# Kernel optimization log

Measured on AMD Instinct MI355X. Metric: run time of the kernel, lower is better.

Reference implementation:

```python
import jax, jax.numpy as jnp
import numpy as np

NU = 100000  # user nodes
NI = 100000  # item nodes
NE = 600000  # edges per etype


def mean_agg(Wh, src, dst, n_dst):
    # copy_u + mean reduce: gather projected src feats, segment-mean over dst
    msg = Wh[src]                                               # [E, d]
    s = jax.ops.segment_sum(msg, dst, num_segments=n_dst)       # [n_dst, d]
    deg = jax.ops.segment_sum(jnp.ones((src.shape[0],), Wh.dtype), dst,
                              num_segments=n_dst)               # [n_dst]
    return s / jnp.maximum(deg, 1.0)[:, None]                   # isolated nodes -> 0


def setup_inputs() -> dict:
    key = jax.random.key(0)
    ks = jax.random.split(key, 20)
    d_in, d_hid, d_out = 128, 128, 16
    inp = {
        'embed_user': jax.random.normal(ks[0], (NU, d_in), jnp.float32),
        'embed_item': jax.random.normal(ks[1], (NI, d_in), jnp.float32),
        'src_uu': jax.random.randint(ks[2], (NE,), 0, NU, jnp.int32),
        'dst_uu': jax.random.randint(ks[3], (NE,), 0, NU, jnp.int32),
        'src_ui': jax.random.randint(ks[4], (NE,), 0, NU, jnp.int32),
        'dst_ui': jax.random.randint(ks[5], (NE,), 0, NI, jnp.int32),
        'src_iu': jax.random.randint(ks[6], (NE,), 0, NI, jnp.int32),
        'dst_iu': jax.random.randint(ks[7], (NE,), 0, NU, jnp.int32),
        'W0_uu': jax.random.normal(ks[8], (d_in, d_hid), jnp.float32) * 0.05,
        'b0_uu': jax.random.normal(ks[9], (d_hid,), jnp.float32) * 0.05,
        'W0_ui': jax.random.normal(ks[10], (d_in, d_hid), jnp.float32) * 0.05,
        'b0_ui': jax.random.normal(ks[11], (d_hid,), jnp.float32) * 0.05,
        'W0_iu': jax.random.normal(ks[12], (d_in, d_hid), jnp.float32) * 0.05,
        'b0_iu': jax.random.normal(ks[13], (d_hid,), jnp.float32) * 0.05,
        'W1_uu': jax.random.normal(ks[14], (d_hid, d_out), jnp.float32) * 0.05,
        'b1_uu': jax.random.normal(ks[15], (d_out,), jnp.float32) * 0.05,
        'W1_ui': jax.random.normal(ks[16], (d_hid, d_out), jnp.float32) * 0.05,
        'b1_ui': jax.random.normal(ks[17], (d_out,), jnp.float32) * 0.05,
        'W1_iu': jax.random.normal(ks[18], (d_hid, d_out), jnp.float32) * 0.05,
        'b1_iu': jax.random.normal(ks[19], (d_out,), jnp.float32) * 0.05,
    }
    return inp


def reference(embed_user, embed_item,
              src_uu, dst_uu, src_ui, dst_ui, src_iu, dst_iu,
              W0_uu, b0_uu, W0_ui, b0_ui, W0_iu, b0_iu,
              W1_uu, b1_uu, W1_ui, b1_ui, W1_iu, b1_iu):
    # Layer 0: per-etype linear, copy_u+mean per etype, sum-combine per dst ntype
    h_user = (mean_agg(embed_user @ W0_uu + b0_uu, src_uu, dst_uu, NU)
              + mean_agg(embed_item @ W0_iu + b0_iu, src_iu, dst_iu, NU))
    h_item = mean_agg(embed_user @ W0_ui + b0_ui, src_ui, dst_ui, NI)
    h_user = jax.nn.relu(h_user)
    h_item = jax.nn.relu(h_item)
    # Layer 1 (dropout p=0): only category='user' output is returned
    out = (mean_agg(h_user @ W1_uu + b1_uu, src_uu, dst_uu, NU)
           + mean_agg(h_item @ W1_iu + b1_iu, src_iu, dst_iu, NU))
    return out
```

## Files before the change

### kernel.cpp

```cpp
#include <hip/hip_runtime.h>
#include <hip/hip_bf16.h>

#define NU 100000
#define NI 100000
#define NEDGE 600000
#define DIN 128
#define DOUT 16
#define NPAD 100032
#define BSH 9
#define NBUCK 196
#define NSB 256
#define SCH 2344

typedef __attribute__((ext_vector_type(8))) short short8;
typedef __attribute__((ext_vector_type(4))) float f32x4;

#define W_EU   0ull
#define W_AUI  6400000ull
#define W_AUU  12802048ull
#define W_AIU  19204096ull
#define W_PW   25606144ull
#define W_OFFU 25632768ull
#define W_OFFI 25732784ull
#define W_OFFX 25832800ull
#define W_SUU  25932816ull
#define W_SIU  26532816ull
#define W_SUI  27132816ull
#define W_EI   27732944ull
#define WS_FULL_BYTES (34132944ull * 4)

__device__ inline unsigned pack_bf16(float x, float y) {
  __hip_bfloat162 h = __float22bfloat162_rn(make_float2(x, y));
  unsigned u;
  __builtin_memcpy(&u, &h, 4);
  return u;
}

__device__ inline short bf16_bits(float x) {
  __hip_bfloat16 h = __float2bfloat16(x);
  short s;
  __builtin_memcpy(&s, &h, 2);
  return s;
}

__device__ inline void bf2_accw(unsigned u, float w, float& ax, float& ay) {
  unsigned lo = u << 16, hi = u & 0xffff0000u;
  float f0, f1;
  __builtin_memcpy(&f0, &lo, 4);
  __builtin_memcpy(&f1, &hi, 4);
  ax = fmaf(f0, w, ax);
  ay = fmaf(f1, w, ay);
}

__global__ __launch_bounds__(256) void prep_kernel(
    const float* __restrict__ Eu, const float* __restrict__ Ei,
    unsigned* __restrict__ Eu_b, unsigned* __restrict__ Ei_b,
    const int* __restrict__ d_uu, const int* __restrict__ d_iu, const int* __restrict__ d_ui,
    int* __restrict__ M,
    const float* __restrict__ W0_uu, const float* __restrict__ W0_ui,
    const float* __restrict__ W0_iu, const float* __restrict__ W1_uu,
    const float* __restrict__ W1_iu, short* __restrict__ pW0_uu, short* __restrict__ pW0_ui,
    short* __restrict__ pW0_iu, short* __restrict__ pW1_uu, short* __restrict__ pW1_iu,
    int nconvU, int nconvI) {
  __shared__ int h[NBUCK];
  int b = blockIdx.x;
  int tid = threadIdx.x;
  if (b < nconvU + nconvI) {
    const float* src;
    unsigned* dst;
    int t;
    if (b < nconvU) { src = Eu; dst = Eu_b; t = b * 256 + tid; }
    else { src = Ei; dst = Ei_b; t = (b - nconvU) * 256 + tid; }
    const float4* s4 = (const float4*)src;
    float4 x = s4[(size_t)t * 2], y = s4[(size_t)t * 2 + 1];
    uint4 o;
    o.x = pack_bf16(x.x, x.y);
    o.y = pack_bf16(x.z, x.w);
    o.z = pack_bf16(y.x, y.y);
    o.w = pack_bf16(y.z, y.w);
    ((uint4*)dst)[t] = o;
    return;
  }
  b -= nconvU + nconvI;
  if (b < 3 * NSB) {
    int t = b / NSB, k = b % NSB;
    if (tid < NBUCK) h[tid] = 0;
    __syncthreads();
    const int* d = (t == 0) ? d_uu : (t == 1) ? d_iu : d_ui;
    int e0 = k * SCH, e1 = min(e0 + SCH, NEDGE);
    for (int e = e0 + tid; e < e1; e += 256) atomicAdd(&h[d[e] >> BSH], 1);
    __syncthreads();
    if (tid < NBUCK) M[t * (NBUCK * NSB) + tid * NSB + k] = h[tid];
    return;
  }
  b -= 3 * NSB;
  int t = b * 256 + tid;
  const float* src;
  short* dst;
  int base;
  bool w1 = false;
  if (t < 16384) { src = W0_uu; dst = pW0_uu; base = t; }
  else if (t < 32768) { src = W0_ui; dst = pW0_ui; base = t - 16384; }
  else if (t < 49152) { src = W0_iu; dst = pW0_iu; base = t - 32768; }
  else if (t < 51200) { src = W1_uu; dst = pW1_uu; base = t - 49152; w1 = true; }
  else if (t < 53248) { src = W1_iu; dst = pW1_iu; base = t - 51200; w1 = true; }
  else return;
  int j = base & 7;
  int lane = (base >> 3) & 63;
  int frag = base >> 9;
  int quad = lane >> 4, l16 = lane & 15;
  float val;
  if (!w1) {
    int kc = frag >> 3, nt = frag & 7;
    val = src[(kc * 32 + quad * 8 + j) * 128 + nt * 16 + l16];
  } else {
    int kc = frag;
    val = src[(kc * 32 + quad * 8 + j) * 16 + l16];
  }
  dst[base] = bf16_bits(val);
}

__global__ __launch_bounds__(256) void scanM_kernel(int* __restrict__ M,
                                                    int* __restrict__ Btot) {
  int t = blockIdx.x / NBUCK, b = blockIdx.x % NBUCK;
  int* Mt = M + t * (NBUCK * NSB) + b * NSB;
  __shared__ int wls[4];
  __shared__ int tot;
  int tid = threadIdx.x, lane = tid & 63, wv = tid >> 6;
  int v = Mt[tid];
  int x = v;
#pragma unroll
  for (int d = 1; d < 64; d <<= 1) {
    int y = __shfl_up(x, d, 64);
    if (lane >= d) x += y;
  }
  if (lane == 63) wls[wv] = x;
  __syncthreads();
  if (tid == 0) {
    int r = 0;
#pragma unroll
    for (int i = 0; i < 4; i++) { int tt = wls[i]; wls[i] = r; r += tt; }
    tot = r;
  }
  __syncthreads();
  Mt[tid] = x - v + wls[wv];
  if (tid == 0) Btot[t * NBUCK + b] = tot;
}

__global__ __launch_bounds__(256) void scanB_kernel(const int* __restrict__ Btot,
                                                    int* __restrict__ Bbase) {
  int t = blockIdx.x;
  __shared__ int wls[4];
  int tid = threadIdx.x, lane = tid & 63, wv = tid >> 6;
  int v = (tid < NBUCK) ? Btot[t * NBUCK + tid] : 0;
  int x = v;
#pragma unroll
  for (int d = 1; d < 64; d <<= 1) {
    int y = __shfl_up(x, d, 64);
    if (lane >= d) x += y;
  }
  if (lane == 63) wls[wv] = x;
  __syncthreads();
  if (tid == 0) {
    int r = 0;
#pragma unroll
    for (int i = 0; i < 4; i++) { int tt = wls[i]; wls[i] = r; r += tt; }
  }
  __syncthreads();
  if (tid < NBUCK) Bbase[t * NBUCK + tid] = x - v + wls[wv];
}

__global__ __launch_bounds__(256) void coarse_scatter_kernel(
    const int* __restrict__ s_uu, const int* __restrict__ d_uu,
    const int* __restrict__ s_iu, const int* __restrict__ d_iu,
    const int* __restrict__ s_ui, const int* __restrict__ d_ui,
    const int* __restrict__ M, const int* __restrict__ Bbase, uint2* __restrict__ pairs) {
  __shared__ int cur[NBUCK];
  int t = blockIdx.x / NSB, k = blockIdx.x % NSB;
  int tid = threadIdx.x;
  if (tid < NBUCK) cur[tid] = M[t * (NBUCK * NSB) + tid * NSB + k] + Bbase[t * NBUCK + tid];
  __syncthreads();
  const int* src = (t == 0) ? s_uu : (t == 1) ? s_iu : s_ui;
  const int* dst = (t == 0) ? d_uu : (t == 1) ? d_iu : d_ui;
  uint2* pr = pairs + (size_t)t * NEDGE;
  int e0 = k * SCH, e1 = min(e0 + SCH, NEDGE);
  for (int e = e0 + tid; e < e1; e += 256) {
    int d = dst[e];
    int pos = atomicAdd(&cur[d >> BSH], 1);
    pr[pos] = make_uint2((unsigned)src[e], (unsigned)d);
  }
}

__global__ __launch_bounds__(256) void fine_sort_kernel(
    const uint2* __restrict__ pairs, const int* __restrict__ Bbase,
    const int* __restrict__ Btot,
    int* __restrict__ off_uu, int* __restrict__ off_iu, int* __restrict__ off_ui,
    int* __restrict__ ssrc_uu, int* __restrict__ ssrc_iu, int* __restrict__ ssrc_ui) {
  __shared__ int h[1 << BSH];
  __shared__ int wls[4];
  int t = blockIdx.x / NBUCK, b = blockIdx.x % NBUCK;
  int tid = threadIdx.x, lane = tid & 63, wv = tid >> 6;
  int* off = (t == 0) ? off_uu : (t == 1) ? off_iu : off_ui;
  int* ss = (t == 0) ? ssrc_uu : (t == 1) ? ssrc_iu : ssrc_ui;
  const uint2* pr = pairs + (size_t)t * NEDGE;
  int base = b << BSH;
  int base_off = Bbase[t * NBUCK + b];
  int cnt = Btot[t * NBUCK + b];
  h[tid] = 0;
  h[tid + 256] = 0;
  __syncthreads();
  for (int e = base_off + tid; e < base_off + cnt; e += 256)
    atomicAdd(&h[(int)pr[e].y - base], 1);
  __syncthreads();
  int h0 = h[2 * tid], h1 = h[2 * tid + 1];
  int s = h0 + h1, x = s;
#pragma unroll
  for (int d = 1; d < 64; d <<= 1) {
    int y = __shfl_up(x, d, 64);
    if (lane >= d) x += y;
  }
  if (lane == 63) wls[wv] = x;
  __syncthreads();
  if (tid == 0) {
    int r = 0;
#pragma unroll
    for (int i = 0; i < 4; i++) { int tt = wls[i]; wls[i] = r; r += tt; }
  }
  __syncthreads();
  int excl = base_off + x - s + wls[wv];
  h[2 * tid] = excl;
  h[2 * tid + 1] = excl + h0;
  __syncthreads();
  int nn = min(1 << BSH, NU - base);
  for (int i = tid; i < nn; i += 256) off[base + i] = h[i];
  if (b == NBUCK - 1 && tid == 0) off[NU] = base_off + cnt;
  __syncthreads();
  for (int e = base_off + tid; e < base_off + cnt; e += 256) {
    uint2 p = pr[e];
    int pos = atomicAdd(&h[(int)p.y - base], 1);
    ss[pos] = (int)p.x;
  }
}

__global__ __launch_bounds__(64, 4) void fused_layer_kernel(
    const uint4* __restrict__ Xu4, const void* __restrict__ Xi, int xi_bf16,
    const int* __restrict__ off_ui, const int* __restrict__ off_uu, const int* __restrict__ off_iu,
    const int* __restrict__ s_ui, const int* __restrict__ s_uu, const int* __restrict__ s_iu,
    const short* __restrict__ pW0_ui, const short* __restrict__ pW0_uu,
    const short* __restrict__ pW0_iu, const float* __restrict__ b0_ui,
    const float* __restrict__ b0_uu, const float* __restrict__ b0_iu,
    const short* __restrict__ pW1_iu, const short* __restrict__ pW1_uu,
    const float* __restrict__ b1_iu, const float* __restrict__ b1_uu,
    float* __restrict__ P_iu, float* __restrict__ P_uu, int nbi) {
  __shared__ __align__(16) float hs[2560];

  const int lane = threadIdx.x;
  const bool user = (int)blockIdx.x < nbi;
  const int blk = user ? (int)blockIdx.x : (int)blockIdx.x - nbi;
  const int rb = blk * 16;

  float* hw = &hs[0];
  uint4* A0 = (uint4*)hw;
  uint4* A1 = A0 + 256;

  {
    const int g = lane >> 4, l16 = lane & 15;
    const int npass = user ? 2 : 1;
#pragma unroll 1
    for (int pass = 0; pass < npass; pass++) {
      const int* off = pass ? off_iu : (user ? off_uu : off_ui);
      const int* ss = pass ? s_iu : (user ? s_uu : s_ui);
      uint4* A = pass ? A1 : A0;
      const bool bf = pass ? (xi_bf16 != 0) : true;
      const uint4* X = pass ? (const uint4*)Xi : Xu4;
      const float4* Xf = (const float4*)Xi;
      if (bf) {
#pragma unroll 1
        for (int ip = 0; ip < 2; ip++) {
          int rA = g * 4 + ip * 2, rB = rA + 1;
          int nodeA = rb + rA, nodeB = rb + rB;
          float acA[8], acB[8];
#pragma unroll
          for (int j = 0; j < 8; j++) { acA[j] = 0.f; acB[j] = 0.f; }
          int s0A = 0, s1A = 0, s0B = 0, s1B = 0;
          if (nodeA < NU) { s0A = off[nodeA]; s1A = off[nodeA + 1]; }
          if (nodeB < NU) { s0B = off[nodeB]; s1B = off[nodeB + 1]; }
          int degA = s1A - s0A, degB = s1B - s0B;
#pragma unroll 1
          for (int eA = s0A, eB = s0B; eA < s1A || eB < s1B; eA += 8, eB += 8) {
            int idxA[8], idxB[8];
            float wtA[8], wtB[8];
#pragma unroll
            for (int j = 0; j < 8; j++) {
              int ea = eA + j, eb = eB + j;
              wtA[j] = (ea < s1A) ? 1.f : 0.f;
              wtB[j] = (eb < s1B) ? 1.f : 0.f;
              idxA[j] = ss[max(min(ea, s1A - 1), 0)];
              idxB[j] = ss[max(min(eb, s1B - 1), 0)];
            }
            uint4 vA[8], vB[8];
#pragma unroll
            for (int j = 0; j < 8; j++) vA[j] = X[(size_t)idxA[j] * 16 + l16];
#pragma unroll
            for (int j = 0; j < 8; j++) vB[j] = X[(size_t)idxB[j] * 16 + l16];
#pragma unroll
            for (int j = 0; j < 8; j++) {
              bf2_accw(vA[j].x, wtA[j], acA[0], acA[1]);
              bf2_accw(vA[j].y, wtA[j], acA[2], acA[3]);
              bf2_accw(vA[j].z, wtA[j], acA[4], acA[5]);
              bf2_accw(vA[j].w, wtA[j], acA[6], acA[7]);
            }
#pragma unroll
            for (int j = 0; j < 8; j++) {
              bf2_accw(vB[j].x, wtB[j], acB[0], acB[1]);
              bf2_accw(vB[j].y, wtB[j], acB[2], acB[3]);
              bf2_accw(vB[j].z, wtB[j], acB[4], acB[5]);
              bf2_accw(vB[j].w, wtB[j], acB[6], acB[7]);
            }
          }
          float invA = 1.0f / fmaxf((float)degA, 1.0f);
          float invB = 1.0f / fmaxf((float)degB, 1.0f);
          uint4 oA, oB;
          oA.x = pack_bf16(acA[0] * invA, acA[1] * invA);
          oA.y = pack_bf16(acA[2] * invA, acA[3] * invA);
          oA.z = pack_bf16(acA[4] * invA, acA[5] * invA);
          oA.w = pack_bf16(acA[6] * invA, acA[7] * invA);
          oB.x = pack_bf16(acB[0] * invB, acB[1] * invB);
          oB.y = pack_bf16(acB[2] * invB, acB[3] * invB);
          oB.z = pack_bf16(acB[4] * invB, acB[5] * invB);
          oB.w = pack_bf16(acB[6] * invB, acB[7] * invB);
          A[rA * 16 + (l16 ^ (rA & 7))] = oA;
          A[rB * 16 + (l16 ^ (rB & 7))] = oB;
        }
      } else {
#pragma unroll 1
        for (int it = 0; it < 4; it++) {
          int r = g * 4 + it;
          int node = rb + r;
          float ac[8];
#pragma unroll
          for (int j = 0; j < 8; j++) ac[j] = 0.f;
          int deg = 0;
          if (node < NU) {
            int s0 = off[node], s1 = off[node + 1];
            deg = s1 - s0;
            if (deg > 0) {
              for (int e = s0; e < s1; e += 4) {
                int idx[4];
                float wt[4];
#pragma unroll
                for (int j = 0; j < 4; j++) {
                  int ee = e + j;
                  bool v = ee < s1;
                  idx[j] = ss[v ? ee : s1 - 1];
                  wt[j] = v ? 1.f : 0.f;
                }
#pragma unroll
                for (int j = 0; j < 4; j++) {
                  float4 pa = Xf[(size_t)idx[j] * 32 + l16 * 2];
                  float4 qa = Xf[(size_t)idx[j] * 32 + l16 * 2 + 1];
                  ac[0] = fmaf(pa.x, wt[j], ac[0]); ac[1] = fmaf(pa.y, wt[j], ac[1]);
                  ac[2] = fmaf(pa.z, wt[j], ac[2]); ac[3] = fmaf(pa.w, wt[j], ac[3]);
                  ac[4] = fmaf(qa.x, wt[j], ac[4]); ac[5] = fmaf(qa.y, wt[j], ac[5]);
                  ac[6] = fmaf(qa.z, wt[j], ac[6]); ac[7] = fmaf(qa.w, wt[j], ac[7]);
                }
              }
            }
          }
          float inv = 1.0f / fmaxf((float)deg, 1.0f);
          uint4 o;
          o.x = pack_bf16(ac[0] * inv, ac[1] * inv);
          o.y = pack_bf16(ac[2] * inv, ac[3] * inv);
          o.z = pack_bf16(ac[4] * inv, ac[5] * inv);
          o.w = pack_bf16(ac[6] * inv, ac[7] * inv);
          A[r * 16 + (l16 ^ (r & 7))] = o;
        }
      }
    }
  }

  const short8* B0p = (const short8*)(user ? pW0_uu : pW0_ui);
  short8 b0pre[8];
#pragma unroll
  for (int nt = 0; nt < 8; nt++) b0pre[nt] = B0p[nt * 64 + lane];

  __syncthreads();

  const int quad = lane >> 4, q16 = lane & 15;
  const int* off0 = user ? off_uu : off_ui;
  const float* b0a = user ? b0_uu : b0_ui;
  const short* W1p = user ? pW1_uu : pW1_iu;
  const float* b1v = user ? b1_uu : b1_iu;
  float* P = user ? P_uu : P_iu;

  float m0[4], m1[4];
#pragma unroll
  for (int r = 0; r < 4; r++) {
    int rr = rb + quad * 4 + r;
    m0[r] = 0.f;
    m1[r] = 0.f;
    if (rr < NU) {
      m0[r] = (off0[rr + 1] > off0[rr]) ? 1.f : 0.f;
      if (user) m1[r] = (off_iu[rr + 1] > off_iu[rr]) ? 1.f : 0.f;
    }
  }

  f32x4 acc[8];
#pragma unroll
  for (int nt = 0; nt < 8; nt++) {
    float ba = b0a[nt * 16 + q16];
    float bb = user ? b0_iu[nt * 16 + q16] : 0.f;
#pragma unroll
    for (int r = 0; r < 4; r++) acc[nt][r] = ba * m0[r] + bb * m1[r];
  }

  const short8* B1p = (const short8*)pW0_iu;
  union u4s8 { uint4 u; short8 s; };
#pragma unroll
  for (int kc = 0; kc < 4; kc++) {
    int c = kc * 4 + quad;
    u4s8 a0, a1;
    a0.u = A0[q16 * 16 + (c ^ (q16 & 7))];
    if (user) a1.u = A1[q16 * 16 + (c ^ (q16 & 7))];
#pragma unroll
    for (int nt = 0; nt < 8; nt++) {
      short8 b0 = (kc == 0) ? b0pre[nt] : B0p[(kc * 8 + nt) * 64 + lane];
      acc[nt] = __builtin_amdgcn_mfma_f32_16x16x32_bf16(a0.s, b0, acc[nt], 0, 0, 0);
      if (user) {
        short8 bb = B1p[(kc * 8 + nt) * 64 + lane];
        acc[nt] = __builtin_amdgcn_mfma_f32_16x16x32_bf16(a1.s, bb, acc[nt], 0, 0, 0);
      }
    }
  }
  __syncthreads();

#pragma unroll
  for (int nt = 0; nt < 8; nt++) {
    int col = nt * 16 + q16;
    float4 v;
    v.x = fmaxf(acc[nt][0], 0.f);
    v.y = fmaxf(acc[nt][1], 0.f);
    v.z = fmaxf(acc[nt][2], 0.f);
    v.w = fmaxf(acc[nt][3], 0.f);
    *(float4*)&hw[col * 20 + quad * 4] = v;
  }
  __syncthreads();

  f32x4 acc2;
  {
    float bv = b1v[q16];
    acc2[0] = bv; acc2[1] = bv; acc2[2] = bv; acc2[3] = bv;
  }
  const short8* W1f = (const short8*)W1p;
#pragma unroll
  for (int kc = 0; kc < 4; kc++) {
    float f[8];
#pragma unroll
    for (int j = 0; j < 8; j++) f[j] = hw[(kc * 32 + quad * 8 + j) * 20 + q16];
    union { uint4 u; short8 s; } hf;
    hf.u.x = pack_bf16(f[0], f[1]);
    hf.u.y = pack_bf16(f[2], f[3]);
    hf.u.z = pack_bf16(f[4], f[5]);
    hf.u.w = pack_bf16(f[6], f[7]);
    short8 bw = W1f[kc * 64 + lane];
    acc2 = __builtin_amdgcn_mfma_f32_16x16x32_bf16(hf.s, bw, acc2, 0, 0, 0);
  }
#pragma unroll
  for (int r = 0; r < 4; r++) {
    int rr = rb + quad * 4 + r;
    if (rr < NU) P[(size_t)rr * DOUT + q16] = acc2[r];
  }
}

__global__ __launch_bounds__(256) void out_kernel(const float4* __restrict__ P_uu,
                                                  const float4* __restrict__ P_iu,
                                                  const int* __restrict__ off_uu,
                                                  const int* __restrict__ s_uu,
                                                  const int* __restrict__ off_iu,
                                                  const int* __restrict__ s_iu,
                                                  float4* __restrict__ out) {
  int w = threadIdx.x >> 6, lane = threadIdx.x & 63;
  int q = lane & 3;
  int sl = (lane >> 2) & 3;
  int nl = lane >> 4;
  int node = blockIdx.x * 16 + w * 4 + nl;
  float4 a = make_float4(0.f, 0.f, 0.f, 0.f);
  float4 b = a;
  int s0 = off_uu[node], s1 = off_uu[node + 1];
  for (int e = s0 + sl; e < s1; e += 16) {
    int idx[4];
    float wt[4];
#pragma unroll
    for (int j = 0; j < 4; j++) {
      int ee = e + j * 4;
      bool v = ee < s1;
      idx[j] = s_uu[v ? ee : s1 - 1];
      wt[j] = v ? 1.f : 0.f;
    }
    float4 vv[4];
#pragma unroll
    for (int j = 0; j < 4; j++) vv[j] = P_uu[(size_t)idx[j] * 4 + q];
#pragma unroll
    for (int j = 0; j < 4; j++) {
      a.x = fmaf(vv[j].x, wt[j], a.x); a.y = fmaf(vv[j].y, wt[j], a.y);
      a.z = fmaf(vv[j].z, wt[j], a.z); a.w = fmaf(vv[j].w, wt[j], a.w);
    }
  }
  int t0 = off_iu[node], t1 = off_iu[node + 1];
  for (int e = t0 + sl; e < t1; e += 16) {
    int idx[4];
    float wt[4];
#pragma unroll
    for (int j = 0; j < 4; j++) {
      int ee = e + j * 4;
      bool v = ee < t1;
      idx[j] = s_iu[v ? ee : t1 - 1];
      wt[j] = v ? 1.f : 0.f;
    }
    float4 vv[4];
#pragma unroll
    for (int j = 0; j < 4; j++) vv[j] = P_iu[(size_t)idx[j] * 4 + q];
#pragma unroll
    for (int j = 0; j < 4; j++) {
      b.x = fmaf(vv[j].x, wt[j], b.x); b.y = fmaf(vv[j].y, wt[j], b.y);
      b.z = fmaf(vv[j].z, wt[j], b.z); b.w = fmaf(vv[j].w, wt[j], b.w);
    }
  }
  float ia = 1.0f / fmaxf((float)(s1 - s0), 1.0f);
  float ib = 1.0f / fmaxf((float)(t1 - t0), 1.0f);
  float4 r;
  r.x = a.x * ia + b.x * ib;
  r.y = a.y * ia + b.y * ib;
  r.z = a.z * ia + b.z * ib;
  r.w = a.w * ia + b.w * ib;
  r.x += __shfl_xor(r.x, 4, 64); r.y += __shfl_xor(r.y, 4, 64);
  r.z += __shfl_xor(r.z, 4, 64); r.w += __shfl_xor(r.w, 4, 64);
  r.x += __shfl_xor(r.x, 8, 64); r.y += __shfl_xor(r.y, 8, 64);
  r.z += __shfl_xor(r.z, 8, 64); r.w += __shfl_xor(r.w, 8, 64);
  if (sl == 0) out[(size_t)node * 4 + q] = r;
}

extern "C" void kernel_launch(void* const* d_in, const int* in_sizes, int n_in,
                              void* d_out, int out_size, void* d_ws, size_t ws_size,
                              hipStream_t stream) {
  (void)in_sizes; (void)n_in; (void)out_size;
  const float* embed_user = (const float*)d_in[0];
  const float* embed_item = (const float*)d_in[1];
  const int* src_uu = (const int*)d_in[2];
  const int* dst_uu = (const int*)d_in[3];
  const int* src_ui = (const int*)d_in[4];
  const int* dst_ui = (const int*)d_in[5];
  const int* src_iu = (const int*)d_in[6];
  const int* dst_iu = (const int*)d_in[7];
  const float* W0_uu = (const float*)d_in[8];
  const float* b0_uu = (const float*)d_in[9];
  const float* W0_ui = (const float*)d_in[10];
  const float* b0_ui = (const float*)d_in[11];
  const float* W0_iu = (const float*)d_in[12];
  const float* b0_iu = (const float*)d_in[13];
  const float* W1_uu = (const float*)d_in[14];
  const float* b1_uu = (const float*)d_in[15];
  const float* W1_iu = (const float*)d_in[18];
  const float* b1_iu = (const float*)d_in[19];
  float* out = (float*)d_out;

  char* ws = (char*)d_ws;
  unsigned* Eu_b = (unsigned*)(ws + W_EU * 4);
  short* pW0_uu = (short*)(ws + W_PW * 4);
  short* pW0_ui = pW0_uu + 16384;
  short* pW0_iu = pW0_uu + 32768;
  short* pW1_uu = pW0_uu + 49152;
  short* pW1_iu = pW0_uu + 51200;
  int* off_uu = (int*)(ws + W_OFFU * 4);
  int* off_iu = (int*)(ws + W_OFFI * 4);
  int* off_ui = (int*)(ws + W_OFFX * 4);
  int* ssrc_uu = (int*)(ws + W_SUU * 4);
  int* ssrc_iu = (int*)(ws + W_SIU * 4);
  int* ssrc_ui = (int*)(ws + W_SUI * 4);
  unsigned* Ei_b = (unsigned*)(ws + W_EI * 4);
  uint2* pairs = (uint2*)(ws + W_AUI * 4);
  int* M = (int*)(ws + W_AUU * 4);
  int* Btot = M + NBUCK * NSB * 3;
  int* Bbase = Btot + NBUCK * 3;
  float* P_iu = (float*)(ws + W_AUU * 4);
  float* P_uu = P_iu + 1600000;

  const int full = (ws_size >= WS_FULL_BYTES) ? 1 : 0;
  const int nconvU = 6250, nconvI = full ? 6250 : 0;
  const void* Xi = full ? (const void*)Ei_b : (const void*)embed_item;

  prep_kernel<<<nconvU + nconvI + 3 * NSB + 208, 256, 0, stream>>>(
      embed_user, embed_item, Eu_b, Ei_b, dst_uu, dst_iu, dst_ui, M,
      W0_uu, W0_ui, W0_iu, W1_uu, W1_iu, pW0_uu, pW0_ui, pW0_iu, pW1_uu, pW1_iu,
      nconvU, nconvI);

  scanM_kernel<<<3 * NBUCK, 256, 0, stream>>>(M, Btot);
  scanB_kernel<<<3, 256, 0, stream>>>(Btot, Bbase);
  coarse_scatter_kernel<<<3 * NSB, 256, 0, stream>>>(src_uu, dst_uu, src_iu, dst_iu,
                                                     src_ui, dst_ui, M, Bbase, pairs);
  fine_sort_kernel<<<3 * NBUCK, 256, 0, stream>>>(pairs, Bbase, Btot,
                                                  off_uu, off_iu, off_ui,
                                                  ssrc_uu, ssrc_iu, ssrc_ui);

  const int nbi = NPAD / 16;
  fused_layer_kernel<<<2 * nbi, 64, 0, stream>>>(
      (const uint4*)Eu_b, Xi, full, off_ui, off_uu, off_iu,
      ssrc_ui, ssrc_uu, ssrc_iu,
      pW0_ui, pW0_uu, pW0_iu, b0_ui, b0_uu, b0_iu,
      pW1_iu, pW1_uu, b1_iu, b1_uu, P_iu, P_uu, nbi);

  out_kernel<<<NU / 16, 256, 0, stream>>>((const float4*)P_uu, (const float4*)P_iu,
                                          off_uu, ssrc_uu, off_iu, ssrc_iu,
                                          (float4*)out);
}
```

Baseline: 339.1 us.

## Merge sort/prep kernels into one cooperative kernel with packed edge pairs

Replaces five separate launches (prep, two scans, coarse scatter, fine sort) with a single cooperative kernel of 768 blocks that uses grid-wide syncs between phases. The conversion and histogram work is done in a grid-stride loop. Edge pairs are also packed into one 32-bit word (local dst offset in the high bits, src in the low 17 bits) instead of a uint2, halving pair traffic. This removes launch gaps and tail effects, at the cost of grid.sync overhead and a fixed grid that may reduce parallelism in the large conversion phase.

```diff
diff --git a/kernel.cpp b/kernel.cpp
--- a/kernel.cpp
+++ b/kernel.cpp
@@ -1,5 +1,8 @@
 #include <hip/hip_runtime.h>
 #include <hip/hip_bf16.h>
+#include <hip/hip_cooperative_groups.h>
+
+namespace cg = cooperative_groups;
 
 #define NU 100000
 #define NI 100000
@@ -11,6 +14,7 @@
 #define NBUCK 196
 #define NSB 256
 #define SCH 2344
+#define SORTGRID 768
 
 typedef __attribute__((ext_vector_type(8))) short short8;
 typedef __attribute__((ext_vector_type(4))) float f32x4;
@@ -52,193 +56,197 @@
   ay = fmaf(f1, w, ay);
 }
 
-__global__ __launch_bounds__(256) void prep_kernel(
+__global__ __launch_bounds__(256) void sortprep_kernel(
     const float* __restrict__ Eu, const float* __restrict__ Ei,
     unsigned* __restrict__ Eu_b, unsigned* __restrict__ Ei_b,
     const int* __restrict__ d_uu, const int* __restrict__ d_iu, const int* __restrict__ d_ui,
-    int* __restrict__ M,
+    const int* __restrict__ s_uu, const int* __restrict__ s_iu, const int* __restrict__ s_ui,
+    int* __restrict__ M, int* __restrict__ Btot, int* __restrict__ Bbase,
+    unsigned* __restrict__ pairs,
+    int* __restrict__ off_uu, int* __restrict__ off_iu, int* __restrict__ off_ui,
+    int* __restrict__ ssrc_uu, int* __restrict__ ssrc_iu, int* __restrict__ ssrc_ui,
     const float* __restrict__ W0_uu, const float* __restrict__ W0_ui,
     const float* __restrict__ W0_iu, const float* __restrict__ W1_uu,
-    const float* __restrict__ W1_iu, short* __restrict__ pW0_uu, short* __restrict__ pW0_ui,
-    short* __restrict__ pW0_iu, short* __restrict__ pW1_uu, short* __restrict__ pW1_iu,
+    const float* __restrict__ W1_iu,
+    short* __restrict__ pW0_uu, short* __restrict__ pW0_ui, short* __restrict__ pW0_iu,
+    short* __restrict__ pW1_uu, short* __restrict__ pW1_iu,
     int nconvU, int nconvI) {
-  __shared__ int h[NBUCK];
-  int b = blockIdx.x;
-  int tid = threadIdx.x;
-  if (b < nconvU + nconvI) {
-    const float* src;
-    unsigned* dst;
-    int t;
-    if (b < nconvU) { src = Eu; dst = Eu_b; t = b * 256 + tid; }
-    else { src = Ei; dst = Ei_b; t = (b - nconvU) * 256 + tid; }
-    const float4* s4 = (const float4*)src;
-    float4 x = s4[(size_t)t * 2], y = s4[(size_t)t * 2 + 1];
-    uint4 o;
-    o.x = pack_bf16(x.x, x.y);
-    o.y = pack_bf16(x.z, x.w);
-    o.z = pack_bf16(y.x, y.y);
-    o.w = pack_bf16(y.z, y.w);
-    ((uint4*)dst)[t] = o;
-    return;
-  }
-  b -= nconvU + nconvI;
-  if (b < 3 * NSB) {
-    int t = b / NSB, k = b % NSB;
-    if (tid < NBUCK) h[tid] = 0;
-    __syncthreads();
-    const int* d = (t == 0) ? d_uu : (t == 1) ? d_iu : d_ui;
+  cg::grid_group grid = cg::this_grid();
+  __shared__ int sh[520];
+  const int tid = threadIdx.x;
+  const int bid = blockIdx.x;
+  const int lane = tid & 63, wv = tid >> 6;
+
+  {
+    const int UC = nconvU + nconvI;
+    const int UH = 3 * NSB;
+    const int UT = UC + UH + 208;
+    for (int u = bid; u < UT; u += SORTGRID) {
+      if (u < UC) {
+        const float* src;
+        unsigned* dst;
+        int t;
+        if (u < nconvU) { src = Eu; dst = Eu_b; t = u * 256 + tid; }
+        else { src = Ei; dst = Ei_b; t = (u - nconvU) * 256 + tid; }
+        const float4* s4 = (const float4*)src;
+        float4 x = s4[(size_t)t * 2], y = s4[(size_t)t * 2 + 1];
+        uint4 o;
+        o.x = pack_bf16(x.x, x.y);
+        o.y = pack_bf16(x.z, x.w);
+        o.z = pack_bf16(y.x, y.y);
+        o.w = pack_bf16(y.z, y.w);
+        ((uint4*)dst)[t] = o;
+      } else if (u < UC + UH) {
+        int b = u - UC;
+        int t = b / NSB, k = b % NSB;
+        if (tid < NBUCK) sh[tid] = 0;
+        __syncthreads();
+        const int* d = (t == 0) ? d_uu : (t == 1) ? d_iu : d_ui;
+        int e0 = k * SCH, e1 = min(e0 + SCH, NEDGE);
+        for (int e = e0 + tid; e < e1; e += 256) atomicAdd(&sh[d[e] >> BSH], 1);
+        __syncthreads();
+        if (tid < NBUCK) M[t * (NBUCK * NSB) + tid * NSB + k] = sh[tid];
+        __syncthreads();
+      } else {
+        int t = (u - UC - UH) * 256 + tid;
+        const float* src;
+        short* dst;
+        int base;
+        bool w1 = false;
+        bool ok = true;
+        if (t < 16384) { src = W0_uu; dst = pW0_uu; base = t; }
+        else if (t < 32768) { src = W0_ui; dst = pW0_ui; base = t - 16384; }
+        else if (t < 49152) { src = W0_iu; dst = pW0_iu; base = t - 32768; }
+        else if (t < 51200) { src = W1_uu; dst = pW1_uu; base = t - 49152; w1 = true; }
+        else if (t < 53248) { src = W1_iu; dst = pW1_iu; base = t - 51200; w1 = true; }
+        else ok = false;
+        if (ok) {
+          int j = base & 7;
+          int ln = (base >> 3) & 63;
+          int frag = base >> 9;
+          int quad = ln >> 4, l16 = ln & 15;
+          float val;
+          if (!w1) {
+            int kc = frag >> 3, nt = frag & 7;
+            val = src[(kc * 32 + quad * 8 + j) * 128 + nt * 16 + l16];
+          } else {
+            int kc = frag;
+            val = src[(kc * 32 + quad * 8 + j) * 16 + l16];
+          }
+          dst[base] = bf16_bits(val);
+        }
+      }
+    }
+  }
+  grid.sync();
+
+  if (bid < 3 * NBUCK) {
+    int t = bid / NBUCK, b = bid % NBUCK;
+    int* Mt = M + t * (NBUCK * NSB) + b * NSB;
+    int* wls = sh + 512;
+    int v = Mt[tid];
+    int x = v;
+#pragma unroll
+    for (int d = 1; d < 64; d <<= 1) {
+      int y = __shfl_up(x, d, 64);
+      if (lane >= d) x += y;
+    }
+    if (lane == 63) wls[wv] = x;
+    __syncthreads();
+    if (tid == 0) {
+      int r = 0;
+#pragma unroll
+      for (int i = 0; i < 4; i++) { int tt = wls[i]; wls[i] = r; r += tt; }
+      sh[516] = r;
+    }
+    __syncthreads();
+    Mt[tid] = x - v + wls[wv];
+    if (tid == 0) Btot[t * NBUCK + b] = sh[516];
+  }
+  grid.sync();
+
+  if (bid < 3) {
+    int t = bid;
+    int* wls = sh + 512;
+    int v = (tid < NBUCK) ? Btot[t * NBUCK + tid] : 0;
+    int x = v;
+#pragma unroll
+    for (int d = 1; d < 64; d <<= 1) {
+      int y = __shfl_up(x, d, 64);
+      if (lane >= d) x += y;
+    }
+    if (lane == 63) wls[wv] = x;
+    __syncthreads();
+    if (tid == 0) {
+      int r = 0;
+#pragma unroll
+      for (int i = 0; i < 4; i++) { int tt = wls[i]; wls[i] = r; r += tt; }
+    }
+    __syncthreads();
+    if (tid < NBUCK) Bbase[t * NBUCK + tid] = x - v + wls[wv];
+  }
+  grid.sync();
+
+  {
+    int t = bid / NSB, k = bid % NSB;
+    if (tid < NBUCK) sh[tid] = M[t * (NBUCK * NSB) + tid * NSB + k] + Bbase[t * NBUCK + tid];
+    __syncthreads();
+    const int* src = (t == 0) ? s_uu : (t == 1) ? s_iu : s_ui;
+    const int* dst = (t == 0) ? d_uu : (t == 1) ? d_iu : d_ui;
+    unsigned* pr = pairs + (size_t)t * NEDGE;
     int e0 = k * SCH, e1 = min(e0 + SCH, NEDGE);
-    for (int e = e0 + tid; e < e1; e += 256) atomicAdd(&h[d[e] >> BSH], 1);
-    __syncthreads();
-    if (tid < NBUCK) M[t * (NBUCK * NSB) + tid * NSB + k] = h[tid];
-    return;
-  }
-  b -= 3 * NSB;
-  int t = b * 256 + tid;
-  const float* src;
-  short* dst;
-  int base;
-  bool w1 = false;
-  if (t < 16384) { src = W0_uu; dst = pW0_uu; base = t; }
-  else if (t < 32768) { src = W0_ui; dst = pW0_ui; base = t - 16384; }
-  else if (t < 49152) { src = W0_iu; dst = pW0_iu; base = t - 32768; }
-  else if (t < 51200) { src = W1_uu; dst = pW1_uu; base = t - 49152; w1 = true; }
-  else if (t < 53248) { src = W1_iu; dst = pW1_iu; base = t - 51200; w1 = true; }
-  else return;
-  int j = base & 7;
-  int lane = (base >> 3) & 63;
-  int frag = base >> 9;
-  int quad = lane >> 4, l16 = lane & 15;
-  float val;
-  if (!w1) {
-    int kc = frag >> 3, nt = frag & 7;
-    val = src[(kc * 32 + quad * 8 + j) * 128 + nt * 16 + l16];
-  } else {
-    int kc = frag;
-    val = src[(kc * 32 + quad * 8 + j) * 16 + l16];
-  }
-  dst[base] = bf16_bits(val);
-}
-
-__global__ __launch_bounds__(256) void scanM_kernel(int* __restrict__ M,
-                                                    int* __restrict__ Btot) {
-  int t = blockIdx.x / NBUCK, b = blockIdx.x % NBUCK;
-  int* Mt = M + t * (NBUCK * NSB) + b * NSB;
-  __shared__ int wls[4];
-  __shared__ int tot;
-  int tid = threadIdx.x, lane = tid & 63, wv = tid >> 6;
-  int v = Mt[tid];
-  int x = v;
-#pragma unroll
-  for (int d = 1; d < 64; d <<= 1) {
-    int y = __shfl_up(x, d, 64);
-    if (lane >= d) x += y;
-  }
-  if (lane == 63) wls[wv] = x;
-  __syncthreads();
-  if (tid == 0) {
-    int r = 0;
-#pragma unroll
-    for (int i = 0; i < 4; i++) { int tt = wls[i]; wls[i] = r; r += tt; }
-    tot = r;
-  }
-  __syncthreads();
-  Mt[tid] = x - v + wls[wv];
-  if (tid == 0) Btot[t * NBUCK + b] = tot;
-}
-
-__global__ __launch_bounds__(256) void scanB_kernel(const int* __restrict__ Btot,
-                                                    int* __restrict__ Bbase) {
-  int t = blockIdx.x;
-  __shared__ int wls[4];
-  int tid = threadIdx.x, lane = tid & 63, wv = tid >> 6;
-  int v = (tid < NBUCK) ? Btot[t * NBUCK + tid] : 0;
-  int x = v;
-#pragma unroll
-  for (int d = 1; d < 64; d <<= 1) {
-    int y = __shfl_up(x, d, 64);
-    if (lane >= d) x += y;
-  }
-  if (lane == 63) wls[wv] = x;
-  __syncthreads();
-  if (tid == 0) {
-    int r = 0;
-#pragma unroll
-    for (int i = 0; i < 4; i++) { int tt = wls[i]; wls[i] = r; r += tt; }
-  }
-  __syncthreads();
-  if (tid < NBUCK) Bbase[t * NBUCK + tid] = x - v + wls[wv];
-}
-
-__global__ __launch_bounds__(256) void coarse_scatter_kernel(
-    const int* __restrict__ s_uu, const int* __restrict__ d_uu,
-    const int* __restrict__ s_iu, const int* __restrict__ d_iu,
-    const int* __restrict__ s_ui, const int* __restrict__ d_ui,
-    const int* __restrict__ M, const int* __restrict__ Bbase, uint2* __restrict__ pairs) {
-  __shared__ int cur[NBUCK];
-  int t = blockIdx.x / NSB, k = blockIdx.x % NSB;
-  int tid = threadIdx.x;
-  if (tid < NBUCK) cur[tid] = M[t * (NBUCK * NSB) + tid * NSB + k] + Bbase[t * NBUCK + tid];
-  __syncthreads();
-  const int* src = (t == 0) ? s_uu : (t == 1) ? s_iu : s_ui;
-  const int* dst = (t == 0) ? d_uu : (t == 1) ? d_iu : d_ui;
-  uint2* pr = pairs + (size_t)t * NEDGE;
-  int e0 = k * SCH, e1 = min(e0 + SCH, NEDGE);
-  for (int e = e0 + tid; e < e1; e += 256) {
-    int d = dst[e];
-    int pos = atomicAdd(&cur[d >> BSH], 1);
-    pr[pos] = make_uint2((unsigned)src[e], (unsigned)d);
-  }
-}
-
-__global__ __launch_bounds__(256) void fine_sort_kernel(
-    const uint2* __restrict__ pairs, const int* __restrict__ Bbase,
-    const int* __restrict__ Btot,
-    int* __restrict__ off_uu, int* __restrict__ off_iu, int* __restrict__ off_ui,
-    int* __restrict__ ssrc_uu, int* __restrict__ ssrc_iu, int* __restrict__ ssrc_ui) {
-  __shared__ int h[1 << BSH];
-  __shared__ int wls[4];
-  int t = blockIdx.x / NBUCK, b = blockIdx.x % NBUCK;
-  int tid = threadIdx.x, lane = tid & 63, wv = tid >> 6;
-  int* off = (t == 0) ? off_uu : (t == 1) ? off_iu : off_ui;
-  int* ss = (t == 0) ? ssrc_uu : (t == 1) ? ssrc_iu : ssrc_ui;
-  const uint2* pr = pairs + (size_t)t * NEDGE;
-  int base = b << BSH;
-  int base_off = Bbase[t * NBUCK + b];
-  int cnt = Btot[t * NBUCK + b];
-  h[tid] = 0;
-  h[tid + 256] = 0;
-  __syncthreads();
-  for (int e = base_off + tid; e < base_off + cnt; e += 256)
-    atomicAdd(&h[(int)pr[e].y - base], 1);
-  __syncthreads();
-  int h0 = h[2 * tid], h1 = h[2 * tid + 1];
-  int s = h0 + h1, x = s;
-#pragma unroll
-  for (int d = 1; d < 64; d <<= 1) {
-    int y = __shfl_up(x, d, 64);
-    if (lane >= d) x += y;
-  }
-  if (lane == 63) wls[wv] = x;
-  __syncthreads();
-  if (tid == 0) {
-    int r = 0;
-#pragma unroll
-    for (int i = 0; i < 4; i++) { int tt = wls[i]; wls[i] = r; r += tt; }
-  }
-  __syncthreads();
-  int excl = base_off + x - s + wls[wv];
-  h[2 * tid] = excl;
-  h[2 * tid + 1] = excl + h0;
-  __syncthreads();
-  int nn = min(1 << BSH, NU - base);
-  for (int i = tid; i < nn; i += 256) off[base + i] = h[i];
-  if (b == NBUCK - 1 && tid == 0) off[NU] = base_off + cnt;
-  __syncthreads();
-  for (int e = base_off + tid; e < base_off + cnt; e += 256) {
-    uint2 p = pr[e];
-    int pos = atomicAdd(&h[(int)p.y - base], 1);
-    ss[pos] = (int)p.x;
+    for (int e = e0 + tid; e < e1; e += 256) {
+      int d = dst[e];
+      int pos = atomicAdd(&sh[d >> BSH], 1);
+      pr[pos] = ((unsigned)(d & ((1 << BSH) - 1)) << 17) | (unsigned)src[e];
+    }
+  }
+  grid.sync();
+
+  if (bid < 3 * NBUCK) {
+    int t = bid / NBUCK, b = bid % NBUCK;
+    int* h = sh;
+    int* wls = sh + 512;
+    int* off = (t == 0) ? off_uu : (t == 1) ? off_iu : off_ui;
+    int* ss = (t == 0) ? ssrc_uu : (t == 1) ? ssrc_iu : ssrc_ui;
+    const unsigned* pr = pairs + (size_t)t * NEDGE;
+    int base = b << BSH;
+    int base_off = Bbase[t * NBUCK + b];
+    int cnt = Btot[t * NBUCK + b];
+    h[tid] = 0;
+    h[tid + 256] = 0;
+    __syncthreads();
+    for (int e = base_off + tid; e < base_off + cnt; e += 256)
+      atomicAdd(&h[pr[e] >> 17], 1);
+    __syncthreads();
+    int h0 = h[2 * tid], h1 = h[2 * tid + 1];
+    int s = h0 + h1, x = s;
+#pragma unroll
+    for (int d = 1; d < 64; d <<= 1) {
+      int y = __shfl_up(x, d, 64);
+      if (lane >= d) x += y;
+    }
+    if (lane == 63) wls[wv] = x;
+    __syncthreads();
+    if (tid == 0) {
+      int r = 0;
+#pragma unroll
+      for (int i = 0; i < 4; i++) { int tt = wls[i]; wls[i] = r; r += tt; }
+    }
+    __syncthreads();
+    int excl = base_off + x - s + wls[wv];
+    h[2 * tid] = excl;
+    h[2 * tid + 1] = excl + h0;
+    __syncthreads();
+    int nn = min(1 << BSH, NU - base);
+    for (int i = tid; i < nn; i += 256) off[base + i] = h[i];
+    if (b == NBUCK - 1 && tid == 0) off[NU] = base_off + cnt;
+    __syncthreads();
+    for (int e = base_off + tid; e < base_off + cnt; e += 256) {
+      unsigned p = pr[e];
+      int pos = atomicAdd(&h[p >> 17], 1);
+      ss[pos] = (int)(p & 0x1FFFFu);
+    }
   }
 }
 
@@ -578,7 +586,7 @@
   int* ssrc_iu = (int*)(ws + W_SIU * 4);
   int* ssrc_ui = (int*)(ws + W_SUI * 4);
   unsigned* Ei_b = (unsigned*)(ws + W_EI * 4);
-  uint2* pairs = (uint2*)(ws + W_AUI * 4);
+  unsigned* pairs = (unsigned*)(ws + W_AUI * 4);
   int* M = (int*)(ws + W_AUU * 4);
   int* Btot = M + NBUCK * NSB * 3;
   int* Bbase = Btot + NBUCK * 3;
@@ -586,21 +594,23 @@
   float* P_uu = P_iu + 1600000;
 
   const int full = (ws_size >= WS_FULL_BYTES) ? 1 : 0;
-  const int nconvU = 6250, nconvI = full ? 6250 : 0;
+  int nconvU = 6250, nconvI = full ? 6250 : 0;
   const void* Xi = full ? (const void*)Ei_b : (const void*)embed_item;
 
-  prep_kernel<<<nconvU + nconvI + 3 * NSB + 208, 256, 0, stream>>>(
-      embed_user, embed_item, Eu_b, Ei_b, dst_uu, dst_iu, dst_ui, M,
-      W0_uu, W0_ui, W0_iu, W1_uu, W1_iu, pW0_uu, pW0_ui, pW0_iu, pW1_uu, pW1_iu,
-      nconvU, nconvI);
-
-  scanM_kernel<<<3 * NBUCK, 256, 0, stream>>>(M, Btot);
-  scanB_kernel<<<3, 256, 0, stream>>>(Btot, Bbase);
-  coarse_scatter_kernel<<<3 * NSB, 256, 0, stream>>>(src_uu, dst_uu, src_iu, dst_iu,
-                                                     src_ui, dst_ui, M, Bbase, pairs);
-  fine_sort_kernel<<<3 * NBUCK, 256, 0, stream>>>(pairs, Bbase, Btot,
-                                                  off_uu, off_iu, off_ui,
-                                                  ssrc_uu, ssrc_iu, ssrc_ui);
+  {
+    void* args[] = {
+        (void*)&embed_user, (void*)&embed_item, (void*)&Eu_b, (void*)&Ei_b,
+        (void*)&dst_uu, (void*)&dst_iu, (void*)&dst_ui,
+        (void*)&src_uu, (void*)&src_iu, (void*)&src_ui,
+        (void*)&M, (void*)&Btot, (void*)&Bbase, (void*)&pairs,
+        (void*)&off_uu, (void*)&off_iu, (void*)&off_ui,
+        (void*)&ssrc_uu, (void*)&ssrc_iu, (void*)&ssrc_ui,
+        (void*)&W0_uu, (void*)&W0_ui, (void*)&W0_iu, (void*)&W1_uu, (void*)&W1_iu,
+        (void*)&pW0_uu, (void*)&pW0_ui, (void*)&pW0_iu, (void*)&pW1_uu, (void*)&pW1_iu,
+        (void*)&nconvU, (void*)&nconvI};
+    hipLaunchCooperativeKernel((const void*)sortprep_kernel, dim3(SORTGRID), dim3(256),
+                               args, 0, stream);
+  }
 
   const int nbi = NPAD / 16;
   fused_layer_kernel<<<2 * nbi, 64, 0, stream>>>(
```

Result: slower. 733.2 us (+116.2%).

## Replace two-pass bucket count/scan with atomic fixed-stride buckets and packed pairs

Applied to the files above, without the earlier changes.

Removes the per-block bucket histogram in prep and the two scan kernels. The scatter kernel now builds its local histogram, reserves slots with a global atomic into fixed-stride (4096) bucket regions, and writes 32-bit packed (local dst, src) entries instead of uint2 pairs. The fine sort kernel does the bucket prefix scan itself and reads from the strided region. This cuts two launches and the pair traffic in half. It assumes no bucket exceeds 4096 edges and that src fits in 17 bits. Edge order within a bucket is now nondeterministic, which can change the order of float sums.

```diff
diff --git a/kernel.cpp b/kernel.cpp
--- a/kernel.cpp
+++ b/kernel.cpp
@@ -11,6 +11,7 @@
 #define NBUCK 196
 #define NSB 256
 #define SCH 2344
+#define BSTRIDE 4096
 
 typedef __attribute__((ext_vector_type(8))) short short8;
 typedef __attribute__((ext_vector_type(4))) float f32x4;
@@ -55,14 +56,12 @@
 __global__ __launch_bounds__(256) void prep_kernel(
     const float* __restrict__ Eu, const float* __restrict__ Ei,
     unsigned* __restrict__ Eu_b, unsigned* __restrict__ Ei_b,
-    const int* __restrict__ d_uu, const int* __restrict__ d_iu, const int* __restrict__ d_ui,
-    int* __restrict__ M,
+    int* __restrict__ bcnt,
     const float* __restrict__ W0_uu, const float* __restrict__ W0_ui,
     const float* __restrict__ W0_iu, const float* __restrict__ W1_uu,
     const float* __restrict__ W1_iu, short* __restrict__ pW0_uu, short* __restrict__ pW0_ui,
     short* __restrict__ pW0_iu, short* __restrict__ pW1_uu, short* __restrict__ pW1_iu,
     int nconvU, int nconvI) {
-  __shared__ int h[NBUCK];
   int b = blockIdx.x;
   int tid = threadIdx.x;
   if (b < nconvU + nconvI) {
@@ -82,18 +81,10 @@
     return;
   }
   b -= nconvU + nconvI;
-  if (b < 3 * NSB) {
-    int t = b / NSB, k = b % NSB;
-    if (tid < NBUCK) h[tid] = 0;
-    __syncthreads();
-    const int* d = (t == 0) ? d_uu : (t == 1) ? d_iu : d_ui;
-    int e0 = k * SCH, e1 = min(e0 + SCH, NEDGE);
-    for (int e = e0 + tid; e < e1; e += 256) atomicAdd(&h[d[e] >> BSH], 1);
-    __syncthreads();
-    if (tid < NBUCK) M[t * (NBUCK * NSB) + tid * NSB + k] = h[tid];
+  if (b == 208) {
+    for (int i = tid; i < 3 * NBUCK; i += 256) bcnt[i] = 0;
     return;
   }
-  b -= 3 * NSB;
   int t = b * 256 + tid;
   const float* src;
   short* dst;
@@ -120,97 +111,73 @@
   dst[base] = bf16_bits(val);
 }
 
-__global__ __launch_bounds__(256) void scanM_kernel(int* __restrict__ M,
-                                                    int* __restrict__ Btot) {
-  int t = blockIdx.x / NBUCK, b = blockIdx.x % NBUCK;
-  int* Mt = M + t * (NBUCK * NSB) + b * NSB;
-  __shared__ int wls[4];
-  __shared__ int tot;
-  int tid = threadIdx.x, lane = tid & 63, wv = tid >> 6;
-  int v = Mt[tid];
-  int x = v;
-#pragma unroll
-  for (int d = 1; d < 64; d <<= 1) {
-    int y = __shfl_up(x, d, 64);
-    if (lane >= d) x += y;
-  }
-  if (lane == 63) wls[wv] = x;
-  __syncthreads();
-  if (tid == 0) {
-    int r = 0;
-#pragma unroll
-    for (int i = 0; i < 4; i++) { int tt = wls[i]; wls[i] = r; r += tt; }
-    tot = r;
-  }
-  __syncthreads();
-  Mt[tid] = x - v + wls[wv];
-  if (tid == 0) Btot[t * NBUCK + b] = tot;
-}
-
-__global__ __launch_bounds__(256) void scanB_kernel(const int* __restrict__ Btot,
-                                                    int* __restrict__ Bbase) {
-  int t = blockIdx.x;
-  __shared__ int wls[4];
-  int tid = threadIdx.x, lane = tid & 63, wv = tid >> 6;
-  int v = (tid < NBUCK) ? Btot[t * NBUCK + tid] : 0;
-  int x = v;
-#pragma unroll
-  for (int d = 1; d < 64; d <<= 1) {
-    int y = __shfl_up(x, d, 64);
-    if (lane >= d) x += y;
-  }
-  if (lane == 63) wls[wv] = x;
-  __syncthreads();
-  if (tid == 0) {
-    int r = 0;
-#pragma unroll
-    for (int i = 0; i < 4; i++) { int tt = wls[i]; wls[i] = r; r += tt; }
-  }
-  __syncthreads();
-  if (tid < NBUCK) Bbase[t * NBUCK + tid] = x - v + wls[wv];
-}
-
-__global__ __launch_bounds__(256) void coarse_scatter_kernel(
+__global__ __launch_bounds__(256) void scatter_kernel(
     const int* __restrict__ s_uu, const int* __restrict__ d_uu,
     const int* __restrict__ s_iu, const int* __restrict__ d_iu,
     const int* __restrict__ s_ui, const int* __restrict__ d_ui,
-    const int* __restrict__ M, const int* __restrict__ Bbase, uint2* __restrict__ pairs) {
+    int* __restrict__ bcnt, unsigned* __restrict__ pairs) {
+  __shared__ int h[NBUCK];
   __shared__ int cur[NBUCK];
   int t = blockIdx.x / NSB, k = blockIdx.x % NSB;
   int tid = threadIdx.x;
-  if (tid < NBUCK) cur[tid] = M[t * (NBUCK * NSB) + tid * NSB + k] + Bbase[t * NBUCK + tid];
-  __syncthreads();
   const int* src = (t == 0) ? s_uu : (t == 1) ? s_iu : s_ui;
   const int* dst = (t == 0) ? d_uu : (t == 1) ? d_iu : d_ui;
-  uint2* pr = pairs + (size_t)t * NEDGE;
+  if (tid < NBUCK) h[tid] = 0;
+  __syncthreads();
   int e0 = k * SCH, e1 = min(e0 + SCH, NEDGE);
+  for (int e = e0 + tid; e < e1; e += 256) atomicAdd(&h[dst[e] >> BSH], 1);
+  __syncthreads();
+  if (tid < NBUCK) {
+    int c = h[tid];
+    int r = (c > 0) ? atomicAdd(&bcnt[t * NBUCK + tid], c) : 0;
+    cur[tid] = t * (NBUCK * BSTRIDE) + tid * BSTRIDE + r;
+  }
+  __syncthreads();
   for (int e = e0 + tid; e < e1; e += 256) {
     int d = dst[e];
     int pos = atomicAdd(&cur[d >> BSH], 1);
-    pr[pos] = make_uint2((unsigned)src[e], (unsigned)d);
+    pairs[pos] = ((unsigned)(d & ((1 << BSH) - 1)) << 17) | (unsigned)src[e];
   }
 }
 
 __global__ __launch_bounds__(256) void fine_sort_kernel(
-    const uint2* __restrict__ pairs, const int* __restrict__ Bbase,
-    const int* __restrict__ Btot,
+    const unsigned* __restrict__ pairs, const int* __restrict__ bcnt,
     int* __restrict__ off_uu, int* __restrict__ off_iu, int* __restrict__ off_ui,
     int* __restrict__ ssrc_uu, int* __restrict__ ssrc_iu, int* __restrict__ ssrc_ui) {
   __shared__ int h[1 << BSH];
   __shared__ int wls[4];
+  __shared__ int pfx[256];
   int t = blockIdx.x / NBUCK, b = blockIdx.x % NBUCK;
   int tid = threadIdx.x, lane = tid & 63, wv = tid >> 6;
   int* off = (t == 0) ? off_uu : (t == 1) ? off_iu : off_ui;
   int* ss = (t == 0) ? ssrc_uu : (t == 1) ? ssrc_iu : ssrc_ui;
-  const uint2* pr = pairs + (size_t)t * NEDGE;
+  {
+    int v = (tid < NBUCK) ? bcnt[t * NBUCK + tid] : 0;
+    int x = v;
+#pragma unroll
+    for (int d = 1; d < 64; d <<= 1) {
+      int y = __shfl_up(x, d, 64);
+      if (lane >= d) x += y;
+    }
+    if (lane == 63) wls[wv] = x;
+    __syncthreads();
+    if (tid == 0) {
+      int r = 0;
+#pragma unroll
+      for (int i = 0; i < 4; i++) { int tt = wls[i]; wls[i] = r; r += tt; }
+    }
+    __syncthreads();
+    pfx[tid] = x - v + wls[wv];
+    __syncthreads();
+  }
   int base = b << BSH;
-  int base_off = Bbase[t * NBUCK + b];
-  int cnt = Btot[t * NBUCK + b];
+  int base_off = pfx[b];
+  int cnt = bcnt[t * NBUCK + b];
+  const unsigned* pr = pairs + (size_t)t * (NBUCK * BSTRIDE) + (size_t)b * BSTRIDE;
   h[tid] = 0;
   h[tid + 256] = 0;
   __syncthreads();
-  for (int e = base_off + tid; e < base_off + cnt; e += 256)
-    atomicAdd(&h[(int)pr[e].y - base], 1);
+  for (int e = tid; e < cnt; e += 256) atomicAdd(&h[pr[e] >> 17], 1);
   __syncthreads();
   int h0 = h[2 * tid], h1 = h[2 * tid + 1];
   int s = h0 + h1, x = s;
@@ -235,10 +202,10 @@
   for (int i = tid; i < nn; i += 256) off[base + i] = h[i];
   if (b == NBUCK - 1 && tid == 0) off[NU] = base_off + cnt;
   __syncthreads();
-  for (int e = base_off + tid; e < base_off + cnt; e += 256) {
-    uint2 p = pr[e];
-    int pos = atomicAdd(&h[(int)p.y - base], 1);
-    ss[pos] = (int)p.x;
+  for (int e = tid; e < cnt; e += 256) {
+    unsigned p = pr[e];
+    int pos = atomicAdd(&h[p >> 17], 1);
+    ss[pos] = (int)(p & 0x1FFFFu);
   }
 }
 
@@ -578,10 +545,8 @@
   int* ssrc_iu = (int*)(ws + W_SIU * 4);
   int* ssrc_ui = (int*)(ws + W_SUI * 4);
   unsigned* Ei_b = (unsigned*)(ws + W_EI * 4);
-  uint2* pairs = (uint2*)(ws + W_AUI * 4);
-  int* M = (int*)(ws + W_AUU * 4);
-  int* Btot = M + NBUCK * NSB * 3;
-  int* Bbase = Btot + NBUCK * 3;
+  unsigned* pairs = (unsigned*)(ws + W_AUI * 4);
+  int* bcnt = (int*)(ws + W_AUU * 4);
   float* P_iu = (float*)(ws + W_AUU * 4);
   float* P_uu = P_iu + 1600000;
 
@@ -589,16 +554,14 @@
   const int nconvU = 6250, nconvI = full ? 6250 : 0;
   const void* Xi = full ? (const void*)Ei_b : (const void*)embed_item;
 
-  prep_kernel<<<nconvU + nconvI + 3 * NSB + 208, 256, 0, stream>>>(
-      embed_user, embed_item, Eu_b, Ei_b, dst_uu, dst_iu, dst_ui, M,
+  prep_kernel<<<nconvU + nconvI + 209, 256, 0, stream>>>(
+      embed_user, embed_item, Eu_b, Ei_b, bcnt,
       W0_uu, W0_ui, W0_iu, W1_uu, W1_iu, pW0_uu, pW0_ui, pW0_iu, pW1_uu, pW1_iu,
       nconvU, nconvI);
 
-  scanM_kernel<<<3 * NBUCK, 256, 0, stream>>>(M, Btot);
-  scanB_kernel<<<3, 256, 0, stream>>>(Btot, Bbase);
-  coarse_scatter_kernel<<<3 * NSB, 256, 0, stream>>>(src_uu, dst_uu, src_iu, dst_iu,
-                                                     src_ui, dst_ui, M, Bbase, pairs);
-  fine_sort_kernel<<<3 * NBUCK, 256, 0, stream>>>(pairs, Bbase, Btot,
+  scatter_kernel<<<3 * NSB, 256, 0, stream>>>(src_uu, dst_uu, src_iu, dst_iu,
+                                              src_ui, dst_ui, bcnt, pairs);
+  fine_sort_kernel<<<3 * NBUCK, 256, 0, stream>>>(pairs, bcnt,
                                                   off_uu, off_iu, off_ui,
                                                   ssrc_uu, ssrc_iu, ssrc_ui);
 
```

Measured after the change: 339.2 us. No clear change (+0.1%).
